# Performance work log

Hardware: AMD Instinct MI355X
Metric: run time of the kernel (lower is better)

The kernel has to match this reference:

```python
import jax, jax.numpy as jnp
import numpy as np

EPS = 1e-5
GROUPS = 8


def setup_inputs() -> dict:
    key = jax.random.key(0)
    ks = jax.random.split(key, 7)
    B, C, L = 16, 512, 4096
    x = jax.random.normal(ks[0], (B, C, L), dtype=jnp.float32)
    gamma = jnp.ones((C,), jnp.float32)
    beta = jnp.zeros((C,), jnp.float32)
    # Conv1d kernel_size=1 weights -> plain matrices
    w1 = jax.random.normal(ks[1], (2 * C, C), jnp.float32) / np.sqrt(C)
    b1 = jax.random.normal(ks[2], (2 * C,), jnp.float32) * 0.01
    w2 = jax.random.normal(ks[3], (C, 2 * C), jnp.float32) / np.sqrt(2 * C)
    b2 = jax.random.normal(ks[4], (C,), jnp.float32) * 0.01
    return {"x": x, "gamma": gamma, "beta": beta, "w1": w1, "b1": b1, "w2": w2, "b2": b2}


def _group_norm(x, gamma, beta):
    B, C, L = x.shape
    xg = x.reshape(B, GROUPS, C // GROUPS, L)
    mean = jnp.mean(xg, axis=(2, 3), keepdims=True)
    var = jnp.var(xg, axis=(2, 3), keepdims=True)
    xn = ((xg - mean) * jax.lax.rsqrt(var + EPS)).reshape(B, C, L)
    return xn * gamma[None, :, None] + beta[None, :, None]


def reference(x, gamma, beta, w1, b1, w2, b2):
    h = _group_norm(x, gamma, beta)                      # [B, C, L]
    h = jnp.einsum('bcl,dc->bdl', h, w1) + b1[None, :, None]  # [B, 2C, L]
    h = jax.nn.gelu(h, approximate=False)
    h = jnp.einsum('bdl,cd->bcl', h, w2) + b2[None, :, None]  # [B, C, L]
    return x + h
```

## Files before the change

### kernel.cpp

```cpp
#include <hip/hip_runtime.h>
#include <cstdint>
#include <cstddef>


typedef unsigned short u16;
typedef unsigned int u32;
typedef __attribute__((ext_vector_type(8))) __bf16 bf16x8;
typedef __attribute__((ext_vector_type(4))) float floatx4;

#define BM 128
#define BN 128
#define BKK 64

__device__ __forceinline__ u16 f2bf(float f) {
    union { float f; u32 u; } v; v.f = f;
    u32 u = v.u;
    return (u16)((u + 0x7fffu + ((u >> 16) & 1u)) >> 16);
}

__device__ __forceinline__ float gelu_exact(float v) {
    const float x = fabsf(v) * 0.70710678118654752f;
    const float t = __builtin_amdgcn_rcpf(fmaf(0.3275911f, x, 1.0f));
    float p = fmaf(1.061405429f, t, -1.453152027f);
    p = fmaf(p, t, 1.421413741f);
    p = fmaf(p, t, -0.284496736f);
    p = fmaf(p, t, 0.254829592f);
    p = p * t;
    const float e = __expf(-x * x);
    const float er = fmaf(-p, e, 1.0f);
    const float s = copysignf(er, v);
    return 0.5f * v * (1.0f + s);
}

__device__ __forceinline__ void async_cp16(u16* lds, const u16* g) {
    __builtin_amdgcn_global_load_lds(
        (const __attribute__((address_space(1))) u32*)g,
        (__attribute__((address_space(3))) u32*)lds,
        16, 0, 0);
}

__global__ __launch_bounds__(256) void gn_stats_partial(const float* __restrict__ x,
                                                        float* __restrict__ pstats) {
    const int bx = blockIdx.x;
    const float4* p = (const float4*)(x + (size_t)(bx >> 3) * 262144 + (size_t)(bx & 7) * 32768);
    float s = 0.f, ss = 0.f;
    for (int i = threadIdx.x; i < 8192; i += 256) {
        float4 v = p[i];
        s += v.x + v.y + v.z + v.w;
        ss += v.x * v.x + v.y * v.y + v.z * v.z + v.w * v.w;
    }
#pragma unroll
    for (int off = 32; off > 0; off >>= 1) {
        s  += __shfl_down(s, off, 64);
        ss += __shfl_down(ss, off, 64);
    }
    __shared__ float rs[8];
    const int wv = threadIdx.x >> 6;
    if ((threadIdx.x & 63) == 0) { rs[wv * 2] = s; rs[wv * 2 + 1] = ss; }
    __syncthreads();
    if (threadIdx.x == 0) {
        pstats[bx * 2]     = rs[0] + rs[2] + rs[4] + rs[6];
        pstats[bx * 2 + 1] = rs[1] + rs[3] + rs[5] + rs[7];
    }
}

__global__ __launch_bounds__(256) void conv_w(const float* __restrict__ w1,
                                              const float* __restrict__ w2,
                                              u16* __restrict__ wb) {
    const int idx = (blockIdx.x * 256 + threadIdx.x) * 4;
    const float4 v = (idx < 524288) ? *(const float4*)(w1 + idx)
                                    : *(const float4*)(w2 + (idx - 524288));
    ushort4 o;
    o.x = f2bf(v.x); o.y = f2bf(v.y); o.z = f2bf(v.z); o.w = f2bf(v.w);
    *(ushort4*)(wb + idx) = o;
}

__global__ __launch_bounds__(256) void gn_norm_tr(const float* __restrict__ x,
                                                  const float* __restrict__ gamma,
                                                  const float* __restrict__ beta,
                                                  const float* __restrict__ pstats,
                                                  u16* __restrict__ xnT, int b0) {
    __shared__ u16 T[4][64][72];
    const int bx = blockIdx.x;
    const int l4 = bx & 15;
    const int ct = (bx >> 4) & 7;
    const int bl = bx >> 7;
    const int b = b0 + bl;
    const int c0 = ct * 64, l0 = l4 * 256;
    const int g = ct;
    float S = 0.f, SS = 0.f;
#pragma unroll
    for (int s2 = 0; s2 < 8; ++s2) {
        S  += pstats[((b * 8 + g) * 8 + s2) * 2];
        SS += pstats[((b * 8 + g) * 8 + s2) * 2 + 1];
    }
    const float inv = 1.f / 262144.f;
    const float mean = S * inv;
    const float var = SS * inv - mean * mean;
    const float rstd = rsqrtf(var + 1e-5f);

    const int t = threadIdx.x;
    const int cl = t >> 3;
    const int lo = (t & 7) * 8;
    const int sw = t & 7;
#pragma unroll
    for (int h = 0; h < 2; ++h) {
        const int c = c0 + cl + h * 32;
        const float sc = rstd * gamma[c];
        const float sh = beta[c] - mean * sc;
        const int ccol = cl + h * 32;
        const int col = (((ccol >> 3) ^ sw) << 3) + (ccol & 7);
        const float* srcr = x + ((size_t)(b * 512 + c) * 4096 + l0 + lo);
#pragma unroll
        for (int q = 0; q < 4; ++q) {
            const float* src = srcr + q * 64;
            float4 a = *(const float4*)src;
            float4 bq = *(const float4*)(src + 4);
            float vv[8] = {a.x, a.y, a.z, a.w, bq.x, bq.y, bq.z, bq.w};
#pragma unroll
            for (int k = 0; k < 8; ++k)
                T[q][lo + k][col] = f2bf(fmaf(vv[k], sc, sh));
        }
    }
    __syncthreads();
    const int ll = t >> 3;
    const int co = (t & 7) * 8, cog = t & 7;
#pragma unroll
    for (int h = 0; h < 2; ++h) {
        const int l = ll + h * 32;
        const int colb = (cog ^ ((l >> 3) & 7)) << 3;
#pragma unroll
        for (int q = 0; q < 4; ++q) {
            const uint4* srcv = (const uint4*)&T[q][l][colb];
            *(uint4*)(xnT + ((size_t)(bl * 4096 + l0 + q * 64 + l) * 512 + c0 + co)) = *srcv;
        }
    }
}

__device__ __forceinline__ void gemm_core(const u16* __restrict__ Ag,
                                          const u16* __restrict__ Bg,
                                          int K, floatx4 acc[4][4],
                                          u16* lA, u16* lB,
                                          int wm, int wn, int fr, int quad) {
    const int t = threadIdx.x;

    auto stage = [&](int buf, int kt) {
        u16* dA = lA + buf * (BM * BKK);
        u16* dB = lB + buf * (BN * BKK);
#pragma unroll
        for (int s = 0; s < 4; ++s) {
            int idx = s * 256 + t;
            int row = idx >> 3;
            int kg = (idx & 7) ^ (row & 7);
            async_cp16(dA + idx * 8, Ag + (size_t)row * K + kt + kg * 8);
        }
#pragma unroll
        for (int s = 0; s < 4; ++s) {
            int idx = s * 256 + t;
            int row = idx >> 3;
            int kg = (idx & 7) ^ (row & 7);
            async_cp16(dB + idx * 8, Bg + (size_t)row * K + kt + kg * 8);
        }
    };

    stage(0, 0);
    __syncthreads();
    int cur = 0;
    for (int kt = 0; kt < K; kt += BKK) {
        if (kt + BKK < K) stage(cur ^ 1, kt + BKK);
        const u16* bA = lA + cur * (BM * BKK);
        const u16* bB = lB + cur * (BN * BKK);
#pragma unroll
        for (int kk = 0; kk < BKK; kk += 32) {
            bf16x8 af[4], bb[4];
#pragma unroll
            for (int i = 0; i < 4; ++i) {
                int row = wm + i * 16 + fr;
                int kg = ((kk >> 3) + quad) ^ (fr & 7);
                af[i] = *(const bf16x8*)(bA + row * BKK + kg * 8);
            }
#pragma unroll
            for (int j = 0; j < 4; ++j) {
                int row = wn + j * 16 + fr;
                int kg = ((kk >> 3) + quad) ^ (fr & 7);
                bb[j] = *(const bf16x8*)(bB + row * BKK + kg * 8);
            }
#pragma unroll
            for (int i = 0; i < 4; ++i)
#pragma unroll
                for (int j = 0; j < 4; ++j)
                    acc[i][j] = __builtin_amdgcn_mfma_f32_16x16x32_bf16(bb[j], af[i], acc[i][j], 0, 0, 0);
        }
        __syncthreads();
        cur ^= 1;
    }
}

__global__ __launch_bounds__(256) void gemm1(const u16* __restrict__ xnT,
                                             const u16* __restrict__ w1b,
                                             const float* __restrict__ b1,
                                             u16* __restrict__ h1T) {
    __shared__ uint4 lAq[2 * BM * BKK / 8], lBq[2 * BN * BKK / 8];
    u16* lA = (u16*)lAq; u16* lB = (u16*)lBq;
    const int bx = blockIdx.x;
    const int nt = (bx >> 3) & 7;
    const int mt = (bx & 7) | ((bx >> 6) << 3);
    const int t = threadIdx.x, lane = t & 63, wv = t >> 6;
    const int wm = (wv & 1) * 64, wn = (wv >> 1) * 64;
    const int fr = lane & 15, quad = lane >> 4;
    floatx4 acc[4][4];
#pragma unroll
    for (int i = 0; i < 4; ++i)
#pragma unroll
        for (int j = 0; j < 4; ++j) acc[i][j] = (floatx4){0.f, 0.f, 0.f, 0.f};

    gemm_core(xnT + (size_t)(mt * BM) * 512, w1b + (size_t)(nt * BN) * 512, 512,
              acc, lA, lB, wm, wn, fr, quad);

    const int mb = mt * BM + wm + fr;
    const int nb = nt * BN + wn + quad * 4;
#pragma unroll
    for (int j = 0; j < 4; ++j) {
        const int n0 = nb + j * 16;
        const float4 bv = *(const float4*)(b1 + n0);
#pragma unroll
        for (int i = 0; i < 4; ++i) {
            const int m = mb + i * 16;
            ushort4 o;
            o.x = f2bf(gelu_exact(acc[i][j][0] + bv.x));
            o.y = f2bf(gelu_exact(acc[i][j][1] + bv.y));
            o.z = f2bf(gelu_exact(acc[i][j][2] + bv.z));
            o.w = f2bf(gelu_exact(acc[i][j][3] + bv.w));
            *(ushort4*)(h1T + (size_t)m * 1024 + n0) = o;
        }
    }
}

__global__ __launch_bounds__(256) void gemm2(const u16* __restrict__ w2b,
                                             const u16* __restrict__ h1T,
                                             const float* __restrict__ b2,
                                             const float* __restrict__ x,
                                             float* __restrict__ out, int b0) {
    __shared__ uint4 lAq[2 * BM * BKK / 8], lBq[2 * BN * BKK / 8];
    u16* lA = (u16*)lAq; u16* lB = (u16*)lBq;
    const int bx = blockIdx.x;
    const int mt = (bx >> 3) & 3;
    const int nt = (bx & 7) | ((bx >> 5) << 3);
    const int t = threadIdx.x, lane = t & 63, wv = t >> 6;
    const int wm = (wv & 1) * 64, wn = (wv >> 1) * 64;
    const int fr = lane & 15, quad = lane >> 4;
    floatx4 acc[4][4];
#pragma unroll
    for (int i = 0; i < 4; ++i)
#pragma unroll
        for (int j = 0; j < 4; ++j) acc[i][j] = (floatx4){0.f, 0.f, 0.f, 0.f};

    gemm_core(w2b + (size_t)(mt * BM) * 1024, h1T + (size_t)(nt * BN) * 1024, 1024,
              acc, lA, lB, wm, wn, fr, quad);

    const int n0g = b0 * 4096 + nt * BN;
    const int b = n0g >> 12;
    const int l_base = n0g & 4095;
    const int mb = mt * BM + wm + fr;
    const int nb = wn + quad * 4;
#pragma unroll
    for (int i = 0; i < 4; ++i) {
        const int m = mb + i * 16;
        const float bv = b2[m];
        const size_t rowoff = ((size_t)(b * 512 + m)) * 4096 + l_base + nb;
#pragma unroll
        for (int j = 0; j < 4; ++j) {
            const float4 xv = *(const float4*)(x + rowoff + j * 16);
            float4 ov;
            ov.x = acc[i][j][0] + bv + xv.x;
            ov.y = acc[i][j][1] + bv + xv.y;
            ov.z = acc[i][j][2] + bv + xv.z;
            ov.w = acc[i][j][3] + bv + xv.w;
            *(float4*)(out + rowoff + j * 16) = ov;
        }
    }
}

extern "C" void kernel_launch(void* const* d_in, const int* in_sizes, int n_in,
                              void* d_out, int out_size, void* d_ws, size_t ws_size,
                              hipStream_t stream) {
    const float* x     = (const float*)d_in[0];
    const float* gamma = (const float*)d_in[1];
    const float* beta  = (const float*)d_in[2];
    const float* w1    = (const float*)d_in[3];
    const float* b1    = (const float*)d_in[4];
    const float* w2    = (const float*)d_in[5];
    const float* b2    = (const float*)d_in[6];
    float* out = (float*)d_out;

    char* ws = (char*)d_ws;
    float* pstats = (float*)ws;
    u16* wb = (u16*)(ws + 65536);
    char* chunkbase = ws + 65536 + (2u << 20);
    const size_t fixed = 65536 + (2u << 20);

    const size_t per = (size_t)192 * 1024 * 1024;
    int NC = 16;
    if      (ws_size >= fixed + per)      NC = 1;
    else if (ws_size >= fixed + per / 2)  NC = 2;
    else if (ws_size >= fixed + per / 4)  NC = 4;
    else if (ws_size >= fixed + per / 8)  NC = 8;
    const int CB = 16 / NC;
    u16* xnT = (u16*)chunkbase;
    u16* h1T = (u16*)(chunkbase + (size_t)CB * 4096 * 512 * 2);

    gn_stats_partial<<<1024, 256, 0, stream>>>(x, pstats);
    conv_w<<<1024, 256, 0, stream>>>(w1, w2, wb);
    for (int ch = 0; ch < NC; ++ch) {
        const int b0 = ch * CB;
        gn_norm_tr<<<CB * 128, 256, 0, stream>>>(x, gamma, beta, pstats, xnT, b0);
        gemm1<<<CB * 32 * 8, 256, 0, stream>>>(xnT, wb, b1, h1T);
        gemm2<<<CB * 32 * 4, 256, 0, stream>>>(wb + 524288, h1T, b2, x, out, b0);
    }
}
```

Baseline: 481.8 us.

## Use register-staged single LDS buffer in GEMMs and fuse stats/weight-convert kernels

Replaces the double-buffered async global-to-LDS copies in the GEMM core with a register prefetch scheme: the next K-tile is loaded into registers while the current single LDS tile is consumed, then written to LDS. This halves LDS usage per block, and launch bounds now request 3 blocks per CU to raise occupancy. The group-norm stats kernel and the weight bf16 conversion kernel are merged into one launch to save a kernel launch. The register staging adds VGPR pressure and an extra barrier per K-step.

```diff
diff --git a/kernel.cpp b/kernel.cpp
--- a/kernel.cpp
+++ b/kernel.cpp
@@ -32,16 +32,21 @@
     return 0.5f * v * (1.0f + s);
 }
 
-__device__ __forceinline__ void async_cp16(u16* lds, const u16* g) {
-    __builtin_amdgcn_global_load_lds(
-        (const __attribute__((address_space(1))) u32*)g,
-        (__attribute__((address_space(3))) u32*)lds,
-        16, 0, 0);
-}
-
-__global__ __launch_bounds__(256) void gn_stats_partial(const float* __restrict__ x,
-                                                        float* __restrict__ pstats) {
+__global__ __launch_bounds__(256) void gn_stats_w(const float* __restrict__ x,
+                                                  float* __restrict__ pstats,
+                                                  const float* __restrict__ w1,
+                                                  const float* __restrict__ w2,
+                                                  u16* __restrict__ wb) {
     const int bx = blockIdx.x;
+    if (bx >= 1024) {
+        const int idx = ((bx - 1024) * 256 + threadIdx.x) * 4;
+        const float4 v = (idx < 524288) ? *(const float4*)(w1 + idx)
+                                        : *(const float4*)(w2 + (idx - 524288));
+        ushort4 o;
+        o.x = f2bf(v.x); o.y = f2bf(v.y); o.z = f2bf(v.z); o.w = f2bf(v.w);
+        *(ushort4*)(wb + idx) = o;
+        return;
+    }
     const float4* p = (const float4*)(x + (size_t)(bx >> 3) * 262144 + (size_t)(bx & 7) * 32768);
     float s = 0.f, ss = 0.f;
     for (int i = threadIdx.x; i < 8192; i += 256) {
@@ -62,17 +67,6 @@
         pstats[bx * 2]     = rs[0] + rs[2] + rs[4] + rs[6];
         pstats[bx * 2 + 1] = rs[1] + rs[3] + rs[5] + rs[7];
     }
-}
-
-__global__ __launch_bounds__(256) void conv_w(const float* __restrict__ w1,
-                                              const float* __restrict__ w2,
-                                              u16* __restrict__ wb) {
-    const int idx = (blockIdx.x * 256 + threadIdx.x) * 4;
-    const float4 v = (idx < 524288) ? *(const float4*)(w1 + idx)
-                                    : *(const float4*)(w2 + (idx - 524288));
-    ushort4 o;
-    o.x = f2bf(v.x); o.y = f2bf(v.y); o.z = f2bf(v.z); o.w = f2bf(v.w);
-    *(ushort4*)(wb + idx) = o;
 }
 
 __global__ __launch_bounds__(256) void gn_norm_tr(const float* __restrict__ x,
@@ -143,33 +137,38 @@
                                           u16* lA, u16* lB,
                                           int wm, int wn, int fr, int quad) {
     const int t = threadIdx.x;
-
-    auto stage = [&](int buf, int kt) {
-        u16* dA = lA + buf * (BM * BKK);
-        u16* dB = lB + buf * (BN * BKK);
-#pragma unroll
-        for (int s = 0; s < 4; ++s) {
-            int idx = s * 256 + t;
-            int row = idx >> 3;
-            int kg = (idx & 7) ^ (row & 7);
-            async_cp16(dA + idx * 8, Ag + (size_t)row * K + kt + kg * 8);
-        }
-#pragma unroll
-        for (int s = 0; s < 4; ++s) {
-            int idx = s * 256 + t;
-            int row = idx >> 3;
-            int kg = (idx & 7) ^ (row & 7);
-            async_cp16(dB + idx * 8, Bg + (size_t)row * K + kt + kg * 8);
-        }
-    };
-
-    stage(0, 0);
-    __syncthreads();
-    int cur = 0;
+    uint4 ra[4], rb[4];
+
+    const u16* sa[4]; const u16* sb[4];
+#pragma unroll
+    for (int s = 0; s < 4; ++s) {
+        const int idx = s * 256 + t;
+        const int row = idx >> 3;
+        const int kg = (idx & 7) ^ (row & 7);
+        sa[s] = Ag + (size_t)row * K + kg * 8;
+        sb[s] = Bg + (size_t)row * K + kg * 8;
+    }
+
+#pragma unroll
+    for (int s = 0; s < 4; ++s) ra[s] = *(const uint4*)(sa[s]);
+#pragma unroll
+    for (int s = 0; s < 4; ++s) rb[s] = *(const uint4*)(sb[s]);
+
     for (int kt = 0; kt < K; kt += BKK) {
-        if (kt + BKK < K) stage(cur ^ 1, kt + BKK);
-        const u16* bA = lA + cur * (BM * BKK);
-        const u16* bB = lB + cur * (BN * BKK);
+#pragma unroll
+        for (int s = 0; s < 4; ++s) *(uint4*)(lA + (s * 256 + t) * 8) = ra[s];
+#pragma unroll
+        for (int s = 0; s < 4; ++s) *(uint4*)(lB + (s * 256 + t) * 8) = rb[s];
+        __syncthreads();
+
+        if (kt + BKK < K) {
+            const int kn = kt + BKK;
+#pragma unroll
+            for (int s = 0; s < 4; ++s) ra[s] = *(const uint4*)(sa[s] + kn);
+#pragma unroll
+            for (int s = 0; s < 4; ++s) rb[s] = *(const uint4*)(sb[s] + kn);
+        }
+
 #pragma unroll
         for (int kk = 0; kk < BKK; kk += 32) {
             bf16x8 af[4], bb[4];
@@ -177,13 +176,13 @@
             for (int i = 0; i < 4; ++i) {
                 int row = wm + i * 16 + fr;
                 int kg = ((kk >> 3) + quad) ^ (fr & 7);
-                af[i] = *(const bf16x8*)(bA + row * BKK + kg * 8);
+                af[i] = *(const bf16x8*)(lA + row * BKK + kg * 8);
             }
 #pragma unroll
             for (int j = 0; j < 4; ++j) {
                 int row = wn + j * 16 + fr;
                 int kg = ((kk >> 3) + quad) ^ (fr & 7);
-                bb[j] = *(const bf16x8*)(bB + row * BKK + kg * 8);
+                bb[j] = *(const bf16x8*)(lB + row * BKK + kg * 8);
             }
 #pragma unroll
             for (int i = 0; i < 4; ++i)
@@ -192,15 +191,14 @@
                     acc[i][j] = __builtin_amdgcn_mfma_f32_16x16x32_bf16(bb[j], af[i], acc[i][j], 0, 0, 0);
         }
         __syncthreads();
-        cur ^= 1;
-    }
-}
-
-__global__ __launch_bounds__(256) void gemm1(const u16* __restrict__ xnT,
-                                             const u16* __restrict__ w1b,
-                                             const float* __restrict__ b1,
-                                             u16* __restrict__ h1T) {
-    __shared__ uint4 lAq[2 * BM * BKK / 8], lBq[2 * BN * BKK / 8];
+    }
+}
+
+__global__ __launch_bounds__(256, 3) void gemm1(const u16* __restrict__ xnT,
+                                                const u16* __restrict__ w1b,
+                                                const float* __restrict__ b1,
+                                                u16* __restrict__ h1T) {
+    __shared__ uint4 lAq[BM * BKK / 8], lBq[BN * BKK / 8];
     u16* lA = (u16*)lAq; u16* lB = (u16*)lBq;
     const int bx = blockIdx.x;
     const int nt = (bx >> 3) & 7;
@@ -236,12 +234,12 @@
     }
 }
 
-__global__ __launch_bounds__(256) void gemm2(const u16* __restrict__ w2b,
-                                             const u16* __restrict__ h1T,
-                                             const float* __restrict__ b2,
-                                             const float* __restrict__ x,
-                                             float* __restrict__ out, int b0) {
-    __shared__ uint4 lAq[2 * BM * BKK / 8], lBq[2 * BN * BKK / 8];
+__global__ __launch_bounds__(256, 3) void gemm2(const u16* __restrict__ w2b,
+                                                const u16* __restrict__ h1T,
+                                                const float* __restrict__ b2,
+                                                const float* __restrict__ x,
+                                                float* __restrict__ out, int b0) {
+    __shared__ uint4 lAq[BM * BKK / 8], lBq[BN * BKK / 8];
     u16* lA = (u16*)lAq; u16* lB = (u16*)lBq;
     const int bx = blockIdx.x;
     const int mt = (bx >> 3) & 3;
@@ -309,8 +307,7 @@
     u16* xnT = (u16*)chunkbase;
     u16* h1T = (u16*)(chunkbase + (size_t)CB * 4096 * 512 * 2);
 
-    gn_stats_partial<<<1024, 256, 0, stream>>>(x, pstats);
-    conv_w<<<1024, 256, 0, stream>>>(w1, w2, wb);
+    gn_stats_w<<<2048, 256, 0, stream>>>(x, pstats, w1, w2, wb);
     for (int ch = 0; ch < NC; ++ch) {
         const int b0 = ch * CB;
         gn_norm_tr<<<CB * 128, 256, 0, stream>>>(x, gamma, beta, pstats, xnT, b0);
```

Result: slower. 1.210 ms (+151.1%).
